# Kernel tuning notes

Hardware: AMD Instinct MI355X
Metric: run time of the kernel (lower is better)

Reference implementation:

```python
import jax, jax.numpy as jnp
import numpy as np

B, T, F, H, O = 4096, 200, 64, 16, 1

def setup_inputs() -> dict:
    key = jax.random.key(0)
    ks = jax.random.split(key, 7)
    s = 1.0 / np.sqrt(H)
    return {
        "input_samples": jax.random.normal(ks[0], (B, T, F), dtype=jnp.float32),
        # LSTM params, PyTorch gate order (i, f, g, o)
        "W_ih": jax.random.uniform(ks[1], (4 * H, F), jnp.float32, -s, s),
        "W_hh": jax.random.uniform(ks[2], (4 * H, H), jnp.float32, -s, s),
        "b_ih": jax.random.uniform(ks[3], (4 * H,), jnp.float32, -s, s),
        "b_hh": jax.random.uniform(ks[4], (4 * H,), jnp.float32, -s, s),
        # final Linear(H -> O)
        "W_out": jax.random.uniform(ks[5], (O, H), jnp.float32, -s, s),
        "b_out": jax.random.uniform(ks[6], (O,), jnp.float32, -s, s),
    }

def reference(input_samples, W_ih, W_hh, b_ih, b_hh, W_out, b_out):
    x = input_samples  # [B, T, F]
    h = W_hh.shape[1]
    # precompute input contribution to gates for all timesteps: [B, T, 4H]
    gx = jnp.einsum('btf,gf->btg', x, W_ih) + b_ih + b_hh

    def step(carry, gx_t):
        h_t, c_t = carry
        g = gx_t + h_t @ W_hh.T  # [B, 4H]
        i, f, gg, o = jnp.split(g, 4, axis=-1)
        i = jax.nn.sigmoid(i)
        f = jax.nn.sigmoid(f)
        gg = jnp.tanh(gg)
        o = jax.nn.sigmoid(o)
        c_new = f * c_t + i * gg
        h_new = o * jnp.tanh(c_new)
        return (h_new, c_new), None

    h0 = jnp.zeros((x.shape[0], h), x.dtype)
    (hT, _cT), _ = jax.lax.scan(step, (h0, h0), jnp.swapaxes(gx, 0, 1))
    # squeeze(h_n) -> [B, H]; Linear + sigmoid -> [B, O]
    return jax.nn.sigmoid(hT @ W_out.T + b_out)
```

## Files before the change

kernel.cpp:

```cpp
#include <hip/hip_runtime.h>


#define Bsz 4096
#define Tn  200
#define Fn  64
#define Hn  16
#define CS  8
#define NCH 25

typedef _Float16 half8  __attribute__((ext_vector_type(8)));
typedef _Float16 half4  __attribute__((ext_vector_type(4)));
typedef float    f32x4  __attribute__((ext_vector_type(4)));

__device__ __forceinline__ half8 to_half8(const float4& a, const float4& b) {
    half8 h;
    h[0] = (_Float16)a.x; h[1] = (_Float16)a.y; h[2] = (_Float16)a.z; h[3] = (_Float16)a.w;
    h[4] = (_Float16)b.x; h[5] = (_Float16)b.y; h[6] = (_Float16)b.z; h[7] = (_Float16)b.w;
    return h;
}

__device__ __forceinline__ float sigm(float z) {
    return __builtin_amdgcn_rcpf(1.0f + __builtin_amdgcn_exp2f(z * -1.4426950408889634f));
}
__device__ __forceinline__ float tanhp(float z) {
    return fmaf(2.0f, __builtin_amdgcn_rcpf(
        1.0f + __builtin_amdgcn_exp2f(z * -2.8853900817779268f)), -1.0f);
}

__global__ __launch_bounds__(192, 1) void lstm_fused(
    const float* __restrict__ x,
    const float* __restrict__ Wih,
    const float* __restrict__ Whh,
    const float* __restrict__ bih,
    const float* __restrict__ bhh,
    const float* __restrict__ Wout,
    const float* __restrict__ bout,
    float* __restrict__ out)
{
    const int lane = threadIdx.x & 63;
    const int wave = threadIdx.x >> 6;
    const int l15  = lane & 15;
    const int lhi  = lane >> 4;
    const int b    = (int)blockIdx.x * 16 + l15;

    __shared__ f32x4 gxbuf[3][CS][4][64];

    half8 WihF[4][2];
    f32x4 biasC[4];
    float4 xr[4][4];
    const int pofs = (wave - 1) * 4;
    const float* xl = x + (size_t)b * (Tn * Fn) + lhi * 8;

    if (wave >= 1) {
#pragma unroll
        for (int m = 0; m < 4; ++m)
#pragma unroll
            for (int kh = 0; kh < 2; ++kh) {
                const float* wr = Wih + (m * 16 + l15) * Fn + kh * 32 + lhi * 8;
                float4 w0 = *reinterpret_cast<const float4*>(wr);
                float4 w1 = *reinterpret_cast<const float4*>(wr + 4);
                WihF[m][kh] = to_half8(w0, w1);
            }
#pragma unroll
        for (int m = 0; m < 4; ++m) {
            float4 v0 = *reinterpret_cast<const float4*>(bih + m * 16 + lhi * 4);
            float4 v1 = *reinterpret_cast<const float4*>(bhh + m * 16 + lhi * 4);
            biasC[m][0] = v0.x + v1.x; biasC[m][1] = v0.y + v1.y;
            biasC[m][2] = v0.z + v1.z; biasC[m][3] = v0.w + v1.w;
        }
#pragma unroll
        for (int s = 0; s < 4; ++s) {
            const float* xp = xl + (pofs + s) * Fn;
            xr[s][0] = *reinterpret_cast<const float4*>(xp);
            xr[s][1] = *reinterpret_cast<const float4*>(xp + 4);
            xr[s][2] = *reinterpret_cast<const float4*>(xp + 32);
            xr[s][3] = *reinterpret_cast<const float4*>(xp + 36);
        }
    }

    half4 WhhHi[4];
#pragma unroll
    for (int m = 0; m < 4; ++m) {
        float4 w = *reinterpret_cast<const float4*>(Whh + (m * 16 + l15) * Hn + lhi * 4);
        WhhHi[m][0] = (_Float16)w.x; WhhHi[m][1] = (_Float16)w.y;
        WhhHi[m][2] = (_Float16)w.z; WhhHi[m][3] = (_Float16)w.w;
    }

    f32x4 cst = { 0.0f, 0.0f, 0.0f, 0.0f };
    half4 hHi = { 0, 0, 0, 0 };
    float hcur[4] = { 0.0f, 0.0f, 0.0f, 0.0f };

    auto recur = [&](f32x4 (&g)[4]) {
        f32x4 pre[4];
#pragma unroll
        for (int m = 0; m < 4; ++m)
            pre[m] = __builtin_amdgcn_mfma_f32_16x16x16f16(WhhHi[m], hHi, g[m], 0, 0, 0);
#pragma unroll
        for (int r = 0; r < 4; ++r) {
            float ig = sigm(pre[0][r]);
            float fg = sigm(pre[1][r]);
            float gg = tanhp(pre[2][r]);
            float og = sigm(pre[3][r]);
            cst[r]  = fmaf(fg, cst[r], ig * gg);
            hcur[r] = og * tanhp(cst[r]);
        }
#pragma unroll
        for (int r = 0; r < 4; ++r)
            hHi[r] = (_Float16)hcur[r];
    };

#pragma unroll 1
    for (int i = 0; i < NCH + 2; ++i) {
        __syncthreads();
        if (wave >= 1) {
            if (i < NCH) {
                const int bi = i % 3;
#pragma unroll
                for (int s = 0; s < 4; ++s) {
                    half8 f0 = to_half8(xr[s][0], xr[s][1]);
                    half8 f1 = to_half8(xr[s][2], xr[s][3]);
#pragma unroll
                    for (int m = 0; m < 4; ++m) {
                        f32x4 acc = __builtin_amdgcn_mfma_f32_16x16x32_f16(
                            WihF[m][0], f0, biasC[m], 0, 0, 0);
                        acc = __builtin_amdgcn_mfma_f32_16x16x32_f16(
                            WihF[m][1], f1, acc, 0, 0, 0);
                        gxbuf[bi][pofs + s][m][lane] = acc;
                    }
                }
                if (i + 1 < NCH) {
                    const float* xc = xl + (size_t)((i + 1) * CS + pofs) * Fn;
#pragma unroll
                    for (int s = 0; s < 4; ++s) {
                        const float* xp = xc + s * Fn;
                        xr[s][0] = *reinterpret_cast<const float4*>(xp);
                        xr[s][1] = *reinterpret_cast<const float4*>(xp + 4);
                        xr[s][2] = *reinterpret_cast<const float4*>(xp + 32);
                        xr[s][3] = *reinterpret_cast<const float4*>(xp + 36);
                    }
                }
            }
        } else {
            if (i >= 2) {
                const int bi = (i - 2) % 3;
                f32x4 gA[4], gB[4];
#pragma unroll
                for (int m = 0; m < 4; ++m) gA[m] = gxbuf[bi][0][m][lane];
#pragma unroll
                for (int m = 0; m < 4; ++m) gB[m] = gxbuf[bi][1][m][lane];
                recur(gA);
#pragma unroll
                for (int m = 0; m < 4; ++m) gA[m] = gxbuf[bi][2][m][lane];
                recur(gB);
#pragma unroll
                for (int m = 0; m < 4; ++m) gB[m] = gxbuf[bi][3][m][lane];
                recur(gA);
#pragma unroll
                for (int m = 0; m < 4; ++m) gA[m] = gxbuf[bi][4][m][lane];
                recur(gB);
#pragma unroll
                for (int m = 0; m < 4; ++m) gB[m] = gxbuf[bi][5][m][lane];
                recur(gA);
#pragma unroll
                for (int m = 0; m < 4; ++m) gA[m] = gxbuf[bi][6][m][lane];
                recur(gB);
#pragma unroll
                for (int m = 0; m < 4; ++m) gB[m] = gxbuf[bi][7][m][lane];
                recur(gA);
                recur(gB);
            }
        }
    }

    if (wave == 0) {
        float4 wo = *reinterpret_cast<const float4*>(Wout + lhi * 4);
        float po = hcur[0] * wo.x;
        po = fmaf(hcur[1], wo.y, po);
        po = fmaf(hcur[2], wo.z, po);
        po = fmaf(hcur[3], wo.w, po);
        po += __shfl_xor(po, 16);
        po += __shfl_xor(po, 32);
        if (lhi == 0)
            out[b] = sigm(po + bout[0]);
    }
}

extern "C" void kernel_launch(void* const* d_in, const int* in_sizes, int n_in,
                              void* d_out, int out_size, void* d_ws, size_t ws_size,
                              hipStream_t stream) {
    const float* x    = (const float*)d_in[0];
    const float* Wih  = (const float*)d_in[1];
    const float* Whh  = (const float*)d_in[2];
    const float* bih  = (const float*)d_in[3];
    const float* bhh  = (const float*)d_in[4];
    const float* Wout = (const float*)d_in[5];
    const float* bout = (const float*)d_in[6];
    float* out = (float*)d_out;

    lstm_fused<<<dim3(Bsz / 16), dim3(192), 0, stream>>>(
        x, Wih, Whh, bih, bhh, Wout, bout, out);
}
```

Measured before the change: 73.71 us.

## Interleave two independent 16-row batch groups in the recurrence wave per block

Each block now handles 32 batch rows instead of 16, with each producer wave computing input projections for its own 16-row group over the full 8-step chunk. The recurrence wave interleaves two independent LSTM chains so that MFMA and transcendental latency of one chain can be hidden behind the other. Buffering drops from triple to double with one barrier per chunk, and x loads for the next chunk are interleaved with the current MFMAs. The grid is halved to 128 blocks, which may leave many CUs idle and lengthens each serial chain's wall time per block.

Result: slower. 127.8 us (+73.3%).

```diff
diff --git a/kernel.cpp b/kernel.cpp
--- a/kernel.cpp
+++ b/kernel.cpp
@@ -37,19 +37,19 @@
     const float* __restrict__ bout,
     float* __restrict__ out)
 {
-    const int lane = threadIdx.x & 63;
-    const int wave = threadIdx.x >> 6;
-    const int l15  = lane & 15;
-    const int lhi  = lane >> 4;
-    const int b    = (int)blockIdx.x * 16 + l15;
+    const int lane  = threadIdx.x & 63;
+    const int wave  = threadIdx.x >> 6;
+    const int l15   = lane & 15;
+    const int lhi   = lane >> 4;
+    const int bbase = (int)blockIdx.x * 32;
 
-    __shared__ f32x4 gxbuf[3][CS][4][64];
+    __shared__ f32x4 gxbuf[2][2][CS][4][64];
 
     half8 WihF[4][2];
     f32x4 biasC[4];
-    float4 xr[4][4];
-    const int pofs = (wave - 1) * 4;
-    const float* xl = x + (size_t)b * (Tn * Fn) + lhi * 8;
+    float4 xr[CS][4];
+    const int pg = (wave >= 1) ? (wave - 1) : 0;
+    const float* xl = x + (size_t)(bbase + pg * 16 + l15) * (Tn * Fn) + lhi * 8;
 
     if (wave >= 1) {
 #pragma unroll
@@ -69,8 +69,8 @@
             biasC[m][2] = v0.z + v1.z; biasC[m][3] = v0.w + v1.w;
         }
 #pragma unroll
-        for (int s = 0; s < 4; ++s) {
-            const float* xp = xl + (pofs + s) * Fn;
+        for (int s = 0; s < CS; ++s) {
+            const float* xp = xl + s * Fn;
             xr[s][0] = *reinterpret_cast<const float4*>(xp);
             xr[s][1] = *reinterpret_cast<const float4*>(xp + 4);
             xr[s][2] = *reinterpret_cast<const float4*>(xp + 32);
@@ -86,102 +86,97 @@
         WhhHi[m][2] = (_Float16)w.z; WhhHi[m][3] = (_Float16)w.w;
     }
 
-    f32x4 cst = { 0.0f, 0.0f, 0.0f, 0.0f };
-    half4 hHi = { 0, 0, 0, 0 };
-    float hcur[4] = { 0.0f, 0.0f, 0.0f, 0.0f };
+    f32x4 cstA = { 0, 0, 0, 0 }, cstB = { 0, 0, 0, 0 };
+    half4 hA = { 0, 0, 0, 0 },   hB = { 0, 0, 0, 0 };
+    float hcA[4] = { 0, 0, 0, 0 }, hcB[4] = { 0, 0, 0, 0 };
 
-    auto recur = [&](f32x4 (&g)[4]) {
+    auto recur = [&](const f32x4 (&g)[4], half4& hh, f32x4& cs, float (&hc)[4]) {
         f32x4 pre[4];
 #pragma unroll
         for (int m = 0; m < 4; ++m)
-            pre[m] = __builtin_amdgcn_mfma_f32_16x16x16f16(WhhHi[m], hHi, g[m], 0, 0, 0);
+            pre[m] = __builtin_amdgcn_mfma_f32_16x16x16f16(WhhHi[m], hh, g[m], 0, 0, 0);
 #pragma unroll
         for (int r = 0; r < 4; ++r) {
             float ig = sigm(pre[0][r]);
             float fg = sigm(pre[1][r]);
             float gg = tanhp(pre[2][r]);
             float og = sigm(pre[3][r]);
-            cst[r]  = fmaf(fg, cst[r], ig * gg);
-            hcur[r] = og * tanhp(cst[r]);
+            cs[r] = fmaf(fg, cs[r], ig * gg);
+            hc[r] = og * tanhp(cs[r]);
         }
 #pragma unroll
         for (int r = 0; r < 4; ++r)
-            hHi[r] = (_Float16)hcur[r];
+            hh[r] = (_Float16)hc[r];
     };
 
 #pragma unroll 1
-    for (int i = 0; i < NCH + 2; ++i) {
-        __syncthreads();
+    for (int i = 0; i <= NCH; ++i) {
         if (wave >= 1) {
             if (i < NCH) {
-                const int bi = i % 3;
+                const int bi  = i & 1;
+                const int cnx = (i + 1 < NCH) ? i + 1 : NCH - 1;
 #pragma unroll
-                for (int s = 0; s < 4; ++s) {
+                for (int s = 0; s < CS; ++s) {
                     half8 f0 = to_half8(xr[s][0], xr[s][1]);
                     half8 f1 = to_half8(xr[s][2], xr[s][3]);
+                    const float* xp = xl + (size_t)(cnx * CS + s) * Fn;
+                    xr[s][0] = *reinterpret_cast<const float4*>(xp);
+                    xr[s][1] = *reinterpret_cast<const float4*>(xp + 4);
+                    xr[s][2] = *reinterpret_cast<const float4*>(xp + 32);
+                    xr[s][3] = *reinterpret_cast<const float4*>(xp + 36);
 #pragma unroll
                     for (int m = 0; m < 4; ++m) {
                         f32x4 acc = __builtin_amdgcn_mfma_f32_16x16x32_f16(
                             WihF[m][0], f0, biasC[m], 0, 0, 0);
                         acc = __builtin_amdgcn_mfma_f32_16x16x32_f16(
                             WihF[m][1], f1, acc, 0, 0, 0);
-                        gxbuf[bi][pofs + s][m][lane] = acc;
-                    }
-                }
-                if (i + 1 < NCH) {
-                    const float* xc = xl + (size_t)((i + 1) * CS + pofs) * Fn;
-#pragma unroll
-                    for (int s = 0; s < 4; ++s) {
-                        const float* xp = xc + s * Fn;
-                        xr[s][0] = *reinterpret_cast<const float4*>(xp);
-                        xr[s][1] = *reinterpret_cast<const float4*>(xp + 4);
-                        xr[s][2] = *reinterpret_cast<const float4*>(xp + 32);
-                        xr[s][3] = *reinterpret_cast<const float4*>(xp + 36);
+                        gxbuf[pg][bi][s][m][lane] = acc;
                     }
                 }
             }
-        } else {
-            if (i >= 2) {
-                const int bi = (i - 2) % 3;
-                f32x4 gA[4], gB[4];
+        } else if (i >= 1) {
+            const int bi = (i - 1) & 1;
+            f32x4 gq[2][2][4];
 #pragma unroll
-                for (int m = 0; m < 4; ++m) gA[m] = gxbuf[bi][0][m][lane];
+            for (int m = 0; m < 4; ++m) {
+                gq[0][0][m] = gxbuf[0][bi][0][m][lane];
+                gq[0][1][m] = gxbuf[1][bi][0][m][lane];
+            }
 #pragma unroll
-                for (int m = 0; m < 4; ++m) gB[m] = gxbuf[bi][1][m][lane];
-                recur(gA);
+            for (int s = 0; s < CS; ++s) {
+                const int cur = s & 1, nxt = cur ^ 1;
+                if (s + 1 < CS) {
 #pragma unroll
-                for (int m = 0; m < 4; ++m) gA[m] = gxbuf[bi][2][m][lane];
-                recur(gB);
-#pragma unroll
-                for (int m = 0; m < 4; ++m) gB[m] = gxbuf[bi][3][m][lane];
-                recur(gA);
-#pragma unroll
-                for (int m = 0; m < 4; ++m) gA[m] = gxbuf[bi][4][m][lane];
-                recur(gB);
-#pragma unroll
-                for (int m = 0; m < 4; ++m) gB[m] = gxbuf[bi][5][m][lane];
-                recur(gA);
-#pragma unroll
-                for (int m = 0; m < 4; ++m) gA[m] = gxbuf[bi][6][m][lane];
-                recur(gB);
-#pragma unroll
-                for (int m = 0; m < 4; ++m) gB[m] = gxbuf[bi][7][m][lane];
-                recur(gA);
-                recur(gB);
+                    for (int m = 0; m < 4; ++m) {
+                        gq[nxt][0][m] = gxbuf[0][bi][s + 1][m][lane];
+                        gq[nxt][1][m] = gxbuf[1][bi][s + 1][m][lane];
+                    }
+                }
+                recur(gq[cur][0], hA, cstA, hcA);
+                recur(gq[cur][1], hB, cstB, hcB);
             }
         }
+        __syncthreads();
     }
 
     if (wave == 0) {
         float4 wo = *reinterpret_cast<const float4*>(Wout + lhi * 4);
-        float po = hcur[0] * wo.x;
-        po = fmaf(hcur[1], wo.y, po);
-        po = fmaf(hcur[2], wo.z, po);
-        po = fmaf(hcur[3], wo.w, po);
-        po += __shfl_xor(po, 16);
-        po += __shfl_xor(po, 32);
-        if (lhi == 0)
-            out[b] = sigm(po + bout[0]);
+        float poA = hcA[0] * wo.x;
+        poA = fmaf(hcA[1], wo.y, poA);
+        poA = fmaf(hcA[2], wo.z, poA);
+        poA = fmaf(hcA[3], wo.w, poA);
+        float poB = hcB[0] * wo.x;
+        poB = fmaf(hcB[1], wo.y, poB);
+        poB = fmaf(hcB[2], wo.z, poB);
+        poB = fmaf(hcB[3], wo.w, poB);
+        poA += __shfl_xor(poA, 16);
+        poA += __shfl_xor(poA, 32);
+        poB += __shfl_xor(poB, 16);
+        poB += __shfl_xor(poB, 32);
+        if (lhi == 0) {
+            out[bbase + l15]      = sigm(poA + bout[0]);
+            out[bbase + 16 + l15] = sigm(poB + bout[0]);
+        }
     }
 }
 
@@ -197,6 +192,6 @@
     const float* bout = (const float*)d_in[6];
     float* out = (float*)d_out;
 
-    lstm_fused<<<dim3(Bsz / 16), dim3(192), 0, stream>>>(
+    lstm_fused<<<dim3(Bsz / 32), dim3(192), 0, stream>>>(
         x, Wih, Whh, bih, bhh, Wout, bout, out);
 }
```
